# Optimization experiments

Measured on AMD Instinct MI355X. Metric: run time of the kernel, lower is better.

Reference implementation:

```python
import jax, jax.numpy as jnp
import numpy as np
from jax.scipy.special import logsumexp

B, C, K = 4096, 8192, 8  # batch, num_classes, positives per sample


def setup_inputs() -> dict:
    key = jax.random.key(0)
    predictions = jax.random.normal(key, (B, C), dtype=jnp.float32)
    # Distinct positive class indices per row (mimics np.setdiff1d assume_unique=True):
    # pairwise diffs within a row are nonzero multiples of 997 with |diff| < C, so distinct mod C.
    labels = (jnp.arange(B, dtype=jnp.int32)[:, None] * 131
              + jnp.arange(K, dtype=jnp.int32)[None, :] * 997) % C
    return {"predictions": predictions, "labels": labels}


def reference(predictions, labels):
    # For each sample b and each positive p in labels[b], the original computes
    # CrossEntropy over the class subset {p} U negatives(b) with target index 0:
    #   term = -pred[b,p] + logsumexp(pred[b,p], pred[b, negatives(b)])
    # Negatives are shared across all positives of a sample, so compute their
    # logsumexp once per row and combine with each positive via logaddexp.
    Bn, Cn = predictions.shape
    rows = jnp.arange(Bn)[:, None]                                   # [B,1]
    pos_mask = jnp.zeros((Bn, Cn), dtype=bool).at[rows, labels].set(True)  # [B,C]
    lse_neg = logsumexp(predictions, axis=-1, where=~pos_mask)       # [B]
    pos_logits = jnp.take_along_axis(predictions, labels, axis=1)    # [B,K]
    loss_terms = jnp.logaddexp(pos_logits, lse_neg[:, None]) - pos_logits  # [B,K]
    # sum over all (sample, positive) pairs, divided by their count
    return jnp.sum(loss_terms) / loss_terms.size
```

## Files before the change

kernel.cpp:

```cpp
#include <hip/hip_runtime.h>


constexpr int B = 4096;
constexpr int C = 8192;
constexpr int K = 8;
constexpr int BLOCK = 256;
constexpr int VPT = C / 4 / BLOCK;

__global__ __launch_bounds__(BLOCK)
void mlsm_row_kernel(const float* __restrict__ pred,
                     const int* __restrict__ labels,
                     float* __restrict__ partial) {
    const int b   = blockIdx.x;
    const int tid = threadIdx.x;
    const float* row = pred + (size_t)b * C;
    const float4* row4 = reinterpret_cast<const float4*>(row);

    float4 v[VPT];
#pragma unroll
    for (int i = 0; i < VPT; ++i)
        v[i] = row4[tid + i * BLOCK];

    float s0 = 0.f, s1 = 0.f, s2 = 0.f, s3 = 0.f;
#pragma unroll
    for (int i = 0; i < VPT; ++i) {
        s0 += __expf(v[i].x);
        s1 += __expf(v[i].y);
        s2 += __expf(v[i].z);
        s3 += __expf(v[i].w);
    }
    float s = (s0 + s1) + (s2 + s3);

#pragma unroll
    for (int off = 32; off > 0; off >>= 1)
        s += __shfl_down(s, off, 64);

    __shared__ float wave_sum[BLOCK / 64];
    if ((tid & 63) == 0) wave_sum[tid >> 6] = s;
    __syncthreads();

    if (tid < K) {
        const float total =
            (wave_sum[0] + wave_sum[1]) + (wave_sum[2] + wave_sum[3]);

        const int cls = labels[b * K + tid];
        const float p = row[cls];
        const float e = __expf(p);

        float sum_pos = e;
#pragma unroll
        for (int m = 1; m < K; m <<= 1)
            sum_pos += __shfl_xor(sum_pos, m, K);

        const float sum_neg = total - sum_pos;
        float term = __logf(e + sum_neg) - p;
#pragma unroll
        for (int m = 1; m < K; m <<= 1)
            term += __shfl_xor(term, m, K);

        if (tid == 0) partial[b] = term;
    }
}

__global__ __launch_bounds__(BLOCK)
void mlsm_reduce_kernel(const float* __restrict__ partial,
                        float* __restrict__ out) {
    const int tid = threadIdx.x;
    const float4* p4 = reinterpret_cast<const float4*>(partial);

    float s = 0.f;
#pragma unroll
    for (int i = 0; i < B / 4 / BLOCK; ++i) {
        float4 v = p4[tid + i * BLOCK];
        s += (v.x + v.y) + (v.z + v.w);
    }
#pragma unroll
    for (int off = 32; off > 0; off >>= 1)
        s += __shfl_down(s, off, 64);

    __shared__ float wave_sum[BLOCK / 64];
    if ((tid & 63) == 0) wave_sum[tid >> 6] = s;
    __syncthreads();

    if (tid == 0)
        out[0] = ((wave_sum[0] + wave_sum[1]) + (wave_sum[2] + wave_sum[3]))
                 * (1.0f / (float)(B * K));
}

extern "C" void kernel_launch(void* const* d_in, const int* in_sizes, int n_in,
                              void* d_out, int out_size, void* d_ws, size_t ws_size,
                              hipStream_t stream) {
    const float* pred = (const float*)d_in[0];
    const int* labels = (const int*)d_in[1];
    float* out        = (float*)d_out;
    float* partial    = (float*)d_ws;

    mlsm_row_kernel<<<B, BLOCK, 0, stream>>>(pred, labels, partial);
    mlsm_reduce_kernel<<<1, BLOCK, 0, stream>>>(partial, out);
}
```

Baseline: 187.2 us.

## Fuse row and final reduction via last-block atomic counter, two rows per block

```diff
diff --git a/kernel.cpp b/kernel.cpp
--- a/kernel.cpp
+++ b/kernel.cpp
@@ -5,46 +5,55 @@
 constexpr int C = 8192;
 constexpr int K = 8;
 constexpr int BLOCK = 256;
+constexpr int RPB = 2;
+constexpr int GRID = B / RPB;
 constexpr int VPT = C / 4 / BLOCK;
 
 __global__ __launch_bounds__(BLOCK)
-void mlsm_row_kernel(const float* __restrict__ pred,
-                     const int* __restrict__ labels,
-                     float* __restrict__ partial) {
-    const int b   = blockIdx.x;
+void mlsm_fused(const float* __restrict__ pred,
+                const int* __restrict__ labels,
+                float* __restrict__ partial,
+                unsigned int* __restrict__ counter,
+                float* __restrict__ out) {
     const int tid = threadIdx.x;
-    const float* row = pred + (size_t)b * C;
-    const float4* row4 = reinterpret_cast<const float4*>(row);
+    __shared__ float wave_sum[RPB][4];
+    __shared__ bool is_last;
 
-    float4 v[VPT];
+    for (int r = 0; r < RPB; ++r) {
+        const int b = blockIdx.x * RPB + r;
+        const float4* row4 =
+            reinterpret_cast<const float4*>(pred + (size_t)b * C);
+
+        float4 v[VPT];
 #pragma unroll
-    for (int i = 0; i < VPT; ++i)
-        v[i] = row4[tid + i * BLOCK];
+        for (int i = 0; i < VPT; ++i)
+            v[i] = row4[tid + i * BLOCK];
 
-    float s0 = 0.f, s1 = 0.f, s2 = 0.f, s3 = 0.f;
+        float s0 = 0.f, s1 = 0.f, s2 = 0.f, s3 = 0.f;
 #pragma unroll
-    for (int i = 0; i < VPT; ++i) {
-        s0 += __expf(v[i].x);
-        s1 += __expf(v[i].y);
-        s2 += __expf(v[i].z);
-        s3 += __expf(v[i].w);
+        for (int i = 0; i < VPT; ++i) {
+            s0 += __expf(v[i].x);
+            s1 += __expf(v[i].y);
+            s2 += __expf(v[i].z);
+            s3 += __expf(v[i].w);
+        }
+        float s = (s0 + s1) + (s2 + s3);
+#pragma unroll
+        for (int off = 32; off > 0; off >>= 1)
+            s += __shfl_down(s, off, 64);
+        if ((tid & 63) == 0) wave_sum[r][tid >> 6] = s;
     }
-    float s = (s0 + s1) + (s2 + s3);
-
-#pragma unroll
-    for (int off = 32; off > 0; off >>= 1)
-        s += __shfl_down(s, off, 64);
-
-    __shared__ float wave_sum[BLOCK / 64];
-    if ((tid & 63) == 0) wave_sum[tid >> 6] = s;
     __syncthreads();
 
-    if (tid < K) {
-        const float total =
-            (wave_sum[0] + wave_sum[1]) + (wave_sum[2] + wave_sum[3]);
+    if (tid < RPB * K) {
+        const int g = tid >> 3;
+        const int k = tid & 7;
+        const int b = blockIdx.x * RPB + g;
+        const float total = (wave_sum[g][0] + wave_sum[g][1]) +
+                            (wave_sum[g][2] + wave_sum[g][3]);
 
-        const int cls = labels[b * K + tid];
-        const float p = row[cls];
+        const int cls = labels[b * K + k];
+        const float p = pred[(size_t)b * C + cls];
         const float e = __expf(p);
 
         float sum_pos = e;
@@ -58,33 +67,35 @@
         for (int m = 1; m < K; m <<= 1)
             term += __shfl_xor(term, m, K);
 
-        if (tid == 0) partial[b] = term;
+        const float other = __shfl(term, 8, 64);
+        if (tid == 0) {
+            partial[blockIdx.x] = term + other;
+            __threadfence();
+            unsigned int old = atomicAdd(counter, 1u);
+            is_last = (old == (unsigned int)(GRID - 1));
+        }
     }
-}
-
-__global__ __launch_bounds__(BLOCK)
-void mlsm_reduce_kernel(const float* __restrict__ partial,
-                        float* __restrict__ out) {
-    const int tid = threadIdx.x;
-    const float4* p4 = reinterpret_cast<const float4*>(partial);
-
-    float s = 0.f;
-#pragma unroll
-    for (int i = 0; i < B / 4 / BLOCK; ++i) {
-        float4 v = p4[tid + i * BLOCK];
-        s += (v.x + v.y) + (v.z + v.w);
-    }
-#pragma unroll
-    for (int off = 32; off > 0; off >>= 1)
-        s += __shfl_down(s, off, 64);
-
-    __shared__ float wave_sum[BLOCK / 64];
-    if ((tid & 63) == 0) wave_sum[tid >> 6] = s;
     __syncthreads();
 
-    if (tid == 0)
-        out[0] = ((wave_sum[0] + wave_sum[1]) + (wave_sum[2] + wave_sum[3]))
-                 * (1.0f / (float)(B * K));
+    if (is_last) {
+        __threadfence();
+        const float4* p4 = reinterpret_cast<const float4*>(partial);
+        float s = 0.f;
+#pragma unroll
+        for (int i = 0; i < GRID / 4 / BLOCK; ++i) {
+            float4 v = p4[tid + i * BLOCK];
+            s += (v.x + v.y) + (v.z + v.w);
+        }
+#pragma unroll
+        for (int off = 32; off > 0; off >>= 1)
+            s += __shfl_down(s, off, 64);
+        if ((tid & 63) == 0) wave_sum[0][tid >> 6] = s;
+        __syncthreads();
+        if (tid == 0)
+            out[0] = ((wave_sum[0][0] + wave_sum[0][1]) +
+                      (wave_sum[0][2] + wave_sum[0][3])) *
+                     (1.0f / (float)(B * K));
+    }
 }
 
 extern "C" void kernel_launch(void* const* d_in, const int* in_sizes, int n_in,
@@ -93,8 +104,11 @@
     const float* pred = (const float*)d_in[0];
     const int* labels = (const int*)d_in[1];
     float* out        = (float*)d_out;
-    float* partial    = (float*)d_ws;
 
-    mlsm_row_kernel<<<B, BLOCK, 0, stream>>>(pred, labels, partial);
-    mlsm_reduce_kernel<<<1, BLOCK, 0, stream>>>(partial, out);
+    float* partial        = (float*)d_ws;
+    unsigned int* counter = (unsigned int*)((char*)d_ws + GRID * sizeof(float));
+
+    hipMemsetAsync(counter, 0, sizeof(unsigned int), stream);
+
+    mlsm_fused<<<GRID, BLOCK, 0, stream>>>(pred, labels, partial, counter, out);
 }
```

New measurement: 279.1 us. 49.1% more time.

## Map one wavefront per row and stream loads in staged chunks

Applied to the files above, without the earlier changes.

```diff
diff --git a/kernel.cpp b/kernel.cpp
--- a/kernel.cpp
+++ b/kernel.cpp
@@ -5,60 +5,59 @@
 constexpr int C = 8192;
 constexpr int K = 8;
 constexpr int BLOCK = 256;
-constexpr int VPT = C / 4 / BLOCK;
+constexpr int RPB = 4;
+constexpr int GRID = B / RPB;
+constexpr int V4_PER_LANE = C / 4 / 64;
+constexpr int STAGE = 8;
 
-__global__ __launch_bounds__(BLOCK)
+__global__ __launch_bounds__(BLOCK, 4)
 void mlsm_row_kernel(const float* __restrict__ pred,
                      const int* __restrict__ labels,
                      float* __restrict__ partial) {
-    const int b   = blockIdx.x;
-    const int tid = threadIdx.x;
+    const int wave = threadIdx.x >> 6;
+    const int lane = threadIdx.x & 63;
+    const int b    = blockIdx.x * RPB + wave;
     const float* row = pred + (size_t)b * C;
     const float4* row4 = reinterpret_cast<const float4*>(row);
 
-    float4 v[VPT];
-#pragma unroll
-    for (int i = 0; i < VPT; ++i)
-        v[i] = row4[tid + i * BLOCK];
+    float p = 0.0f;
+    if (lane < K) p = row[labels[b * K + lane]];
 
     float s0 = 0.f, s1 = 0.f, s2 = 0.f, s3 = 0.f;
 #pragma unroll
-    for (int i = 0; i < VPT; ++i) {
-        s0 += __expf(v[i].x);
-        s1 += __expf(v[i].y);
-        s2 += __expf(v[i].z);
-        s3 += __expf(v[i].w);
+    for (int g = 0; g < V4_PER_LANE / STAGE; ++g) {
+        float4 v[STAGE];
+#pragma unroll
+        for (int i = 0; i < STAGE; ++i)
+            v[i] = row4[lane + (g * STAGE + i) * 64];
+#pragma unroll
+        for (int i = 0; i < STAGE; ++i) {
+            s0 += __expf(v[i].x);
+            s1 += __expf(v[i].y);
+            s2 += __expf(v[i].z);
+            s3 += __expf(v[i].w);
+        }
     }
     float s = (s0 + s1) + (s2 + s3);
 
 #pragma unroll
-    for (int off = 32; off > 0; off >>= 1)
-        s += __shfl_down(s, off, 64);
+    for (int m = 1; m < 64; m <<= 1)
+        s += __shfl_xor(s, m, 64);
 
-    __shared__ float wave_sum[BLOCK / 64];
-    if ((tid & 63) == 0) wave_sum[tid >> 6] = s;
-    __syncthreads();
-
-    if (tid < K) {
-        const float total =
-            (wave_sum[0] + wave_sum[1]) + (wave_sum[2] + wave_sum[3]);
-
-        const int cls = labels[b * K + tid];
-        const float p = row[cls];
+    if (lane < K) {
         const float e = __expf(p);
-
         float sum_pos = e;
 #pragma unroll
         for (int m = 1; m < K; m <<= 1)
             sum_pos += __shfl_xor(sum_pos, m, K);
 
-        const float sum_neg = total - sum_pos;
+        const float sum_neg = s - sum_pos;
         float term = __logf(e + sum_neg) - p;
 #pragma unroll
         for (int m = 1; m < K; m <<= 1)
             term += __shfl_xor(term, m, K);
 
-        if (tid == 0) partial[b] = term;
+        if (lane == 0) partial[b] = term;
     }
 }
 
@@ -95,6 +94,6 @@
     float* out        = (float*)d_out;
     float* partial    = (float*)d_ws;
 
-    mlsm_row_kernel<<<B, BLOCK, 0, stream>>>(pred, labels, partial);
+    mlsm_row_kernel<<<GRID, BLOCK, 0, stream>>>(pred, labels, partial);
     mlsm_reduce_kernel<<<1, BLOCK, 0, stream>>>(partial, out);
 }
```

Measured after the change: 187.7 us. Within noise of the previous version (+0.3%).
